# Performance work log

Hardware: AMD Instinct MI355X
Metric: run time of the kernel (lower is better)

The kernel has to match this reference:

```python
import jax, jax.numpy as jnp
import numpy as np

EPS = 1e-6
SIGMA = 1.0       # get_matrix default sigma
INIT_SIGMA = 1.0  # args.init_sigma


def setup_inputs() -> dict:
    key = jax.random.key(0)
    ks = jax.random.split(key, 12)
    B, T, LD, NB = 16, 2048, 256, 32
    s = 1.0 / np.sqrt(LD)
    E_raw = jax.random.normal(ks[5], (LD, LD), jnp.float32)
    E_w, _ = jnp.linalg.qr(E_raw)  # orthogonal like geotorch.orthogonal
    return {
        "Z": jax.random.normal(ks[0], (B, T, LD), jnp.float32),
        "obs_times": jax.random.uniform(ks[1], (B, T, 1), jnp.float32),
        "D": jax.random.normal(ks[2], (NB, LD), jnp.float32),
        "coeff_W": jax.random.normal(ks[3], (NB, LD), jnp.float32) * s,
        "coeff_b": jnp.zeros((NB,), jnp.float32),
        "E_w": E_w.astype(jnp.float32),
        "B_w": jax.random.normal(ks[6], (LD, LD), jnp.float32) * s,
        "C_w": jax.random.normal(ks[7], (LD, LD), jnp.float32) * s,
        "M_w": jax.random.normal(ks[8], (LD, LD), jnp.float32) * s,
        "init_mean_p": jax.random.normal(ks[9], (LD,), jnp.float32),
        "init_log_var": jax.random.normal(ks[10], (LD,), jnp.float32),
        "y_log_var": jax.random.normal(ks[11], (LD,), jnp.float32),
    }


def _binop(qi, qj):
    # (A_j*A_i, Bu_j + A_j*Bu_i): combine earlier element qi with later qj
    A_i, Bu_i = qi
    A_j, Bu_j = qj
    return (A_j * A_i, Bu_j + A_j * Bu_i)


def reference(Z, obs_times, D, coeff_W, coeff_b, E_w, B_w, C_w, M_w,
              init_mean_p, init_log_var, y_log_var):
    LD = Z.shape[-1]
    # alphas = B(Z)
    alphas = jnp.einsum('btd,ed->bte', Z, B_w)                      # (B,T,LD)
    # get_matrix (vectorized over batch and time)
    A_basis = -(jnp.exp(D) + EPS)                                   # (NB,LD), negative
    A_coeff = jax.nn.softmax(jnp.einsum('btd,nd->btn', alphas, coeff_W) + coeff_b, axis=-1)
    A_mat = jnp.einsum('btn,nd->btd', A_coeff, A_basis)             # (B,T,LD)
    exp_A_m = jnp.exp(A_mat * obs_times)                            # mean transition
    exp_B_m = (exp_A_m - 1.0) / A_mat * alphas
    exp_A_v = jnp.exp(2.0 * A_mat * obs_times)                      # var transition
    exp_B_v = 0.5 * SIGMA ** 2 * (exp_A_v - 1.0) / A_mat + EPS
    mats_A = jnp.concatenate([exp_A_m, exp_A_v], axis=-1)           # (B,T,2LD)
    mats_B = jnp.concatenate([exp_B_m, exp_B_v], axis=-1)           # (B,T,2LD)
    # parallel linear-recurrence scan over time
    cum_A, cum_B = jax.lax.associative_scan(_binop, (mats_A, mats_B), axis=1)
    # initial condition in rotated coordinates
    init_mean0 = E_w.T @ init_mean_p                                # (LD,)
    diag_v = INIT_SIGMA * (jnp.exp(init_log_var) + EPS)
    init_var0 = jnp.einsum('ki,k->i', E_w ** 2, diag_v)             # diag(E^T diag(v) E)
    init_mv = jnp.concatenate([init_mean0, init_var0], axis=0)      # (2LD,)
    imv = cum_A * init_mv                                           # (B,T,2LD)
    init_mean, init_var = imv[..., :LD], imv[..., LD:]
    xs_mean, xs_var = cum_B[..., :LD], cum_B[..., LD:]
    y_var = jnp.exp(y_log_var) + EPS
    # output projections: M(E(.)) and history C(E(Z))
    history = jnp.einsum('btd,ed,fe->btf', Z, E_w, C_w)
    means = jnp.einsum('btd,ed,fe->btf', xs_mean + init_mean, E_w, M_w) + history
    stds = jnp.einsum('btd,ed,fe->btf', jnp.sqrt(xs_var + init_var + y_var), E_w, M_w)
    return means, stds, alphas
```

## Files before the change

### kernel.cpp

```cpp
#include <hip/hip_runtime.h>
#include <math.h>

#define EPS 1e-6f

#define B_   16
#define T_   2048
#define LD   256
#define NB   32
#define BT   (B_ * T_)
#define NCH  32
#define CHUNK (T_ / NCH)

typedef short bf16x8 __attribute__((ext_vector_type(8)));
typedef float f32x4  __attribute__((ext_vector_type(4)));

__device__ __forceinline__ unsigned short f2b(float f) {
    unsigned int u = __float_as_uint(f);
    unsigned int r = (u + 0x7fffu + ((u >> 16) & 1u)) >> 16;
    return (unsigned short)r;
}

__device__ __forceinline__ void gl_lds16(const void* g, void* l) {
    __builtin_amdgcn_global_load_lds(
        (const __attribute__((address_space(1))) unsigned int*)g,
        (__attribute__((address_space(3))) unsigned int*)l, 16, 0, 0);
}

__device__ __forceinline__ void stage_tile(const unsigned short* __restrict__ src,
                                           int row0, int stride, int kb,
                                           unsigned short* lds, int wv, int lane) {
#pragma unroll
    for (int cc = 0; cc < 2; ++cc) {
        int c = wv * 2 + cc;
        int r = c * 16 + (lane >> 2);
        int qd = (lane & 3) ^ ((r >> 1) & 3);
        const unsigned short* g = src + (size_t)(row0 + r) * stride + kb + qd * 8;
        gl_lds16(g, lds + c * 512);
    }
}

__device__ __forceinline__ bf16x8 frag_ld(const unsigned short* lds, int row, int qd) {
    int pq = qd ^ ((row >> 1) & 3);
    return *(const bf16x8*)(lds + row * 32 + pq * 8);
}

template<int KLEN, int HALVES, int DUAL>
__global__ __launch_bounds__(256) void k_gemm128(const unsigned short* __restrict__ A0,
                                                 const unsigned short* __restrict__ A1,
                                                 const unsigned short* __restrict__ B0,
                                                 const unsigned short* __restrict__ B1,
                                                 float* __restrict__ C,
                                                 unsigned short* __restrict__ C2,
                                                 int nout) {
    __shared__ unsigned short As[128 * 32];
    __shared__ unsigned short Bs[128 * 32];
    int tid = threadIdx.x, lane = tid & 63, wv = tid >> 6;
    int m0 = blockIdx.x * 128, n0 = blockIdx.y * 128;
    int wm = (wv & 1) * 64, wn = (wv >> 1) * 64;
    f32x4 acc[4][4];
#pragma unroll
    for (int i = 0; i < 4; ++i)
#pragma unroll
        for (int j = 0; j < 4; ++j) acc[i][j] = (f32x4){0.f, 0.f, 0.f, 0.f};

    for (int h = 0; h < HALVES; ++h) {
        const unsigned short* A = h ? A1 : A0;
        const unsigned short* B = h ? B1 : B0;
        for (int kb = 0; kb < KLEN; kb += 32) {
            stage_tile(A, m0, KLEN, kb, As, wv, lane);
            stage_tile(B, n0, KLEN, kb, Bs, wv, lane);
            __syncthreads();
            int qd = lane >> 4;
            bf16x8 af[4], bf[4];
#pragma unroll
            for (int i = 0; i < 4; ++i) af[i] = frag_ld(As, wm + i * 16 + (lane & 15), qd);
#pragma unroll
            for (int j = 0; j < 4; ++j) bf[j] = frag_ld(Bs, wn + j * 16 + (lane & 15), qd);
#pragma unroll
            for (int i = 0; i < 4; ++i)
#pragma unroll
                for (int j = 0; j < 4; ++j)
                    acc[i][j] = __builtin_amdgcn_mfma_f32_16x16x32_bf16(af[i], bf[j], acc[i][j], 0, 0, 0);
            __syncthreads();
        }
    }
    int col = wn + (lane & 15);
    int rb  = wm + ((lane >> 4) << 2);
#pragma unroll
    for (int i = 0; i < 4; ++i)
#pragma unroll
        for (int j = 0; j < 4; ++j)
#pragma unroll
            for (int r = 0; r < 4; ++r) {
                int row = m0 + rb + i * 16 + r;
                int cc  = n0 + col + j * 16;
                float v = acc[i][j][r];
                C[(size_t)row * nout + cc] = v;
                if (DUAL) C2[(size_t)row * nout + cc] = f2b(v);
            }
}

__global__ __launch_bounds__(256) void k_gemm_logits(const unsigned short* __restrict__ A,
                                                     const unsigned short* __restrict__ B,
                                                     const float* __restrict__ bias,
                                                     float* __restrict__ C) {
    __shared__ unsigned short As[128 * 32];
    __shared__ unsigned short Bs2[32 * 32];
    int tid = threadIdx.x, lane = tid & 63, wv = tid >> 6;
    int m0 = blockIdx.x * 128;
    f32x4 acc[2][2];
#pragma unroll
    for (int i = 0; i < 2; ++i)
#pragma unroll
        for (int j = 0; j < 2; ++j) acc[i][j] = (f32x4){0.f, 0.f, 0.f, 0.f};

    for (int kb = 0; kb < 256; kb += 32) {
        stage_tile(A, m0, 256, kb, As, wv, lane);
        if (wv < 2) {
            int r = wv * 16 + (lane >> 2);
            int qd = (lane & 3) ^ ((r >> 1) & 3);
            gl_lds16(B + (size_t)r * 256 + kb + qd * 8, Bs2 + wv * 512);
        }
        __syncthreads();
        int qd = lane >> 4;
        bf16x8 af[2], bff[2];
#pragma unroll
        for (int i = 0; i < 2; ++i) af[i] = frag_ld(As, wv * 32 + i * 16 + (lane & 15), qd);
#pragma unroll
        for (int j = 0; j < 2; ++j) bff[j] = frag_ld(Bs2, j * 16 + (lane & 15), qd);
#pragma unroll
        for (int i = 0; i < 2; ++i)
#pragma unroll
            for (int j = 0; j < 2; ++j)
                acc[i][j] = __builtin_amdgcn_mfma_f32_16x16x32_bf16(af[i], bff[j], acc[i][j], 0, 0, 0);
        __syncthreads();
    }
    int col = lane & 15;
    int rb  = (lane >> 4) << 2;
#pragma unroll
    for (int i = 0; i < 2; ++i)
#pragma unroll
        for (int j = 0; j < 2; ++j)
#pragma unroll
            for (int r = 0; r < 4; ++r) {
                int row = m0 + wv * 32 + i * 16 + rb + r;
                int cc  = j * 16 + col;
                C[(size_t)row * NB + cc] = acc[i][j][r] + bias[cc];
            }
}

__global__ void k_cast(const float* __restrict__ src, unsigned short* __restrict__ dst, int n4) {
    int i = blockIdx.x * blockDim.x + threadIdx.x;
    if (i < n4) {
        float4 v = ((const float4*)src)[i];
        ushort4 o = make_ushort4(f2b(v.x), f2b(v.y), f2b(v.z), f2b(v.w));
        ((ushort4*)dst)[i] = o;
    }
}

__global__ void k_small_gemm(const float* __restrict__ E, const float* __restrict__ W,
                             unsigned short* __restrict__ out) {
    __shared__ float Ws[16][17];
    __shared__ float Es[16][17];
    int tx = threadIdx.x, ty = threadIdx.y;
    int d0 = blockIdx.x * 16, f0 = blockIdx.y * 16;
    float acc = 0.f;
    for (int eb = 0; eb < LD; eb += 16) {
        Ws[ty][tx] = W[(f0 + ty) * LD + eb + tx];
        Es[ty][tx] = E[(eb + ty) * LD + d0 + tx];
        __syncthreads();
#pragma unroll
        for (int k = 0; k < 16; ++k) acc = fmaf(Ws[ty][k], Es[k][tx], acc);
        __syncthreads();
    }
    out[(f0 + ty) * LD + d0 + tx] = f2b(acc);
}

__global__ void k_vec_pre(const float* __restrict__ E, const float* __restrict__ imp,
                          const float* __restrict__ ilv, const float* __restrict__ ylv,
                          const float* __restrict__ Dm,
                          float* __restrict__ im0, float* __restrict__ iv0,
                          float* __restrict__ yv, unsigned short* __restrict__ AbT) {
    int t = threadIdx.x;
    if (blockIdx.x == 0) {
        float sm = 0.f, sv = 0.f;
        for (int k = 0; k < LD; ++k) {
            float e = E[k * LD + t];
            sm = fmaf(e, imp[k], sm);
            sv = fmaf(e * e, expf(ilv[k]) + EPS, sv);
        }
        im0[t] = sm;
        iv0[t] = sv;
        yv[t]  = expf(ylv[t]) + EPS;
    } else {
        int n = blockIdx.x - 1;
        AbT[t * NB + n] = f2b(-(expf(Dm[n * LD + t]) + EPS));
    }
}

__global__ __launch_bounds__(256) void k_soft(const float* __restrict__ logits,
                                              unsigned short* __restrict__ ach) {
    int tid = threadIdx.x;
    int row = blockIdx.x * 8 + (tid >> 5);
    int l = tid & 31;
    float v = logits[(size_t)row * NB + l];
    float mx = v;
#pragma unroll
    for (int off = 16; off >= 1; off >>= 1) mx = fmaxf(mx, __shfl_xor(mx, off, 32));
    float e = expf(v - mx);
    float s = e;
#pragma unroll
    for (int off = 16; off >= 1; off >>= 1) s += __shfl_xor(s, off, 32);
    ach[(size_t)row * NB + l] = f2b(e / s);
}

__global__ __launch_bounds__(256) void k_tot(const float* __restrict__ Amat,
                                             const float* __restrict__ alphas,
                                             const float* __restrict__ obs,
                                             float* __restrict__ totA,
                                             float* __restrict__ totBm,
                                             float* __restrict__ totBv) {
    int d = threadIdx.x;
    int b = blockIdx.x >> 5, ch = blockIdx.x & 31;
    int bt0 = b * T_ + ch * CHUNK;
    float ra = 1.f, rm = 0.f, rv = 0.f;
    for (int i = 0; i < CHUNK; ++i) {
        size_t idx = (size_t)(bt0 + i) * LD + d;
        float Am = Amat[idx];
        float av = alphas[idx];
        float tt = obs[bt0 + i];
        float eAm = expf(Am * tt);
        float ieA = 1.f / Am;
        float eBm = (eAm - 1.f) * ieA * av;
        float eBv = 0.5f * (eAm * eAm - 1.f) * ieA + EPS;
        rm = fmaf(eAm, rm, eBm);
        rv = fmaf(eAm * eAm, rv, eBv);
        ra *= eAm;
    }
    int pidx = blockIdx.x * LD + d;
    totA[pidx] = ra; totBm[pidx] = rm; totBv[pidx] = rv;
}

__global__ void k_chunkpfx(const float* __restrict__ totA, const float* __restrict__ totBm,
                           const float* __restrict__ totBv,
                           float* __restrict__ preA, float* __restrict__ preBm,
                           float* __restrict__ preBv) {
    int d = threadIdx.x;
    int b = blockIdx.x;
    float Pa = 1.f, Pm = 0.f, Pv = 0.f;
    for (int ch = 0; ch < NCH; ++ch) {
        int pidx = (b * NCH + ch) * LD + d;
        preA[pidx] = Pa; preBm[pidx] = Pm; preBv[pidx] = Pv;
        float a = totA[pidx], tm_ = totBm[pidx], tv = totBv[pidx];
        Pm = fmaf(a, Pm, tm_);
        Pv = fmaf(a * a, Pv, tv);
        Pa = a * Pa;
    }
}

__global__ __launch_bounds__(256) void k_scan_apply(const float* __restrict__ Amat,
                                                    const float* __restrict__ alphas,
                                                    const float* __restrict__ obs,
                                                    const float* __restrict__ preA,
                                                    const float* __restrict__ preBm,
                                                    const float* __restrict__ preBv,
                                                    const float* __restrict__ im0,
                                                    const float* __restrict__ iv0,
                                                    const float* __restrict__ yv,
                                                    unsigned short* __restrict__ Mh,
                                                    unsigned short* __restrict__ Sh) {
    int d = threadIdx.x;
    int b = blockIdx.x >> 5, ch = blockIdx.x & 31;
    int bt0 = b * T_ + ch * CHUNK;
    int pidx = blockIdx.x * LD + d;
    float ga = preA[pidx], gm = preBm[pidx], gv = preBv[pidx];
    float i0 = im0[d], v0 = iv0[d], yvd = yv[d];
    for (int i = 0; i < CHUNK; ++i) {
        size_t idx = (size_t)(bt0 + i) * LD + d;
        float Am = Amat[idx];
        float av = alphas[idx];
        float tt = obs[bt0 + i];
        float eAm = expf(Am * tt);
        float ieA = 1.f / Am;
        float eBm = (eAm - 1.f) * ieA * av;
        float eBv = 0.5f * (eAm * eAm - 1.f) * ieA + EPS;
        gm = fmaf(eAm, gm, eBm);
        gv = fmaf(eAm * eAm, gv, eBv);
        ga *= eAm;
        float mm = fmaf(ga, i0, gm);
        float vv = fmaf(ga * ga, v0, gv) + yvd;
        Mh[idx] = f2b(mm);
        Sh[idx] = f2b(sqrtf(vv));
    }
}

extern "C" void kernel_launch(void* const* d_in, const int* in_sizes, int n_in,
                              void* d_out, int out_size, void* d_ws, size_t ws_size,
                              hipStream_t stream) {
    const float* Z   = (const float*)d_in[0];
    const float* obs = (const float*)d_in[1];
    const float* Dm  = (const float*)d_in[2];
    const float* cw  = (const float*)d_in[3];
    const float* cb  = (const float*)d_in[4];
    const float* Ew  = (const float*)d_in[5];
    const float* Bw  = (const float*)d_in[6];
    const float* Cw  = (const float*)d_in[7];
    const float* Mw  = (const float*)d_in[8];
    const float* imp = (const float*)d_in[9];
    const float* ilv = (const float*)d_in[10];
    const float* ylv = (const float*)d_in[11];

    float* out    = (float*)d_out;
    float* means  = out;
    float* stds   = out + (size_t)BT * LD;
    float* alphas = out + (size_t)2 * BT * LD;

    unsigned short* Zh = (unsigned short*)stds;

    char* ws = (char*)d_ws;
    size_t o = 0;
    float*          Amat = (float*)(ws + o);          o += (size_t)BT * LD * 4;
    unsigned short* Mh   = (unsigned short*)(ws + o); o += (size_t)BT * LD * 2;
    unsigned short* Sh   = (unsigned short*)(ws + o); o += (size_t)BT * LD * 2;
    unsigned short* ach  = (unsigned short*)(ws + o); o += (size_t)BT * NB * 2;
    unsigned short* GMh  = (unsigned short*)(ws + o); o += (size_t)LD * LD * 2;
    unsigned short* GCh  = (unsigned short*)(ws + o); o += (size_t)LD * LD * 2;
    unsigned short* Bwh  = (unsigned short*)(ws + o); o += (size_t)LD * LD * 2;
    unsigned short* cwh  = (unsigned short*)(ws + o); o += (size_t)NB * LD * 2;
    unsigned short* AbT  = (unsigned short*)(ws + o); o += (size_t)LD * NB * 2;
    float* totA  = (float*)(ws + o); o += (size_t)B_ * NCH * LD * 4;
    float* totBm = (float*)(ws + o); o += (size_t)B_ * NCH * LD * 4;
    float* totBv = (float*)(ws + o); o += (size_t)B_ * NCH * LD * 4;
    float* preA  = (float*)(ws + o); o += (size_t)B_ * NCH * LD * 4;
    float* preBm = (float*)(ws + o); o += (size_t)B_ * NCH * LD * 4;
    float* preBv = (float*)(ws + o); o += (size_t)B_ * NCH * LD * 4;
    float* im0   = (float*)(ws + o); o += LD * 4;
    float* iv0   = (float*)(ws + o); o += LD * 4;
    float* yv    = (float*)(ws + o); o += LD * 4;

    unsigned short* alphash = Mh;
    float*          logits  = (float*)Sh;

    k_cast<<<dim3((BT * LD / 4 + 255) / 256), dim3(256), 0, stream>>>(Z, Zh, BT * LD / 4);
    k_cast<<<dim3((LD * LD / 4 + 255) / 256), dim3(256), 0, stream>>>(Bw, Bwh, LD * LD / 4);
    k_cast<<<dim3((NB * LD / 4 + 255) / 256), dim3(256), 0, stream>>>(cw, cwh, NB * LD / 4);
    k_small_gemm<<<dim3(16, 16), dim3(16, 16), 0, stream>>>(Ew, Mw, GMh);
    k_small_gemm<<<dim3(16, 16), dim3(16, 16), 0, stream>>>(Ew, Cw, GCh);
    k_vec_pre<<<dim3(33), dim3(LD), 0, stream>>>(Ew, imp, ilv, ylv, Dm, im0, iv0, yv, AbT);

    k_gemm128<256, 1, 1><<<dim3(BT / 128, 2), dim3(256), 0, stream>>>(
        Zh, nullptr, Bwh, nullptr, alphas, alphash, LD);

    k_gemm_logits<<<dim3(BT / 128), dim3(256), 0, stream>>>(alphash, cwh, cb, logits);
    k_soft<<<dim3(BT / 8), dim3(256), 0, stream>>>(logits, ach);
    k_gemm128<32, 1, 0><<<dim3(BT / 128, 2), dim3(256), 0, stream>>>(
        ach, nullptr, AbT, nullptr, Amat, nullptr, LD);

    k_tot<<<dim3(B_ * NCH), dim3(LD), 0, stream>>>(Amat, alphas, obs, totA, totBm, totBv);
    k_chunkpfx<<<dim3(B_), dim3(LD), 0, stream>>>(totA, totBm, totBv, preA, preBm, preBv);
    k_scan_apply<<<dim3(B_ * NCH), dim3(LD), 0, stream>>>(Amat, alphas, obs,
                                                          preA, preBm, preBv,
                                                          im0, iv0, yv, Mh, Sh);

    k_gemm128<256, 2, 0><<<dim3(BT / 128, 2), dim3(256), 0, stream>>>(
        Mh, Zh, GMh, GCh, means, nullptr, LD);
    k_gemm128<256, 1, 0><<<dim3(BT / 128, 2), dim3(256), 0, stream>>>(
        Sh, nullptr, GMh, nullptr, stds, nullptr, LD);
}
```

Baseline: 288.9 us.

## Fold B_w into coeff_W, fuse prep kernels, recompute A_mat inside scan

Collapses the setup casts, small GEMMs and vector prep into one multi-role launch, and precomputes coeff_W·B_w so the logits come straight from Z. The logits GEMM then runs in the same launch as the alphas GEMM. Softmax and the A_mat contraction are recomputed in the two scan kernels from logits held in LDS, so the fp32 A_mat tensor is never written to or read from global memory. The means and stds GEMMs are merged into a single launch. This cuts launches and large intermediate traffic, at the cost of redundant softmax and 32-term dot products in each scan pass and a changed rounding path for the logits.

```diff
diff --git a/kernel.cpp b/kernel.cpp
--- a/kernel.cpp
+++ b/kernel.cpp
@@ -44,31 +44,95 @@
     return *(const bf16x8*)(lds + row * 32 + pq * 8);
 }
 
-template<int KLEN, int HALVES, int DUAL>
-__global__ __launch_bounds__(256) void k_gemm128(const unsigned short* __restrict__ A0,
-                                                 const unsigned short* __restrict__ A1,
-                                                 const unsigned short* __restrict__ B0,
-                                                 const unsigned short* __restrict__ B1,
-                                                 float* __restrict__ C,
-                                                 unsigned short* __restrict__ C2,
-                                                 int nout) {
+__global__ __launch_bounds__(256) void k_pre(const float* __restrict__ Z,
+                                             const float* __restrict__ Dm,
+                                             const float* __restrict__ cw,
+                                             const float* __restrict__ Ew,
+                                             const float* __restrict__ Bw,
+                                             const float* __restrict__ Cw,
+                                             const float* __restrict__ Mw,
+                                             const float* __restrict__ imp,
+                                             const float* __restrict__ ilv,
+                                             const float* __restrict__ ylv,
+                                             unsigned short* __restrict__ GMh,
+                                             unsigned short* __restrict__ GCh,
+                                             unsigned short* __restrict__ cwbh,
+                                             float* __restrict__ im0,
+                                             float* __restrict__ iv0,
+                                             float* __restrict__ yv,
+                                             float* __restrict__ Ab,
+                                             unsigned short* __restrict__ Bwh,
+                                             unsigned short* __restrict__ Zh) {
+    int bid = blockIdx.x;
+    int tid = threadIdx.x;
+    if (bid < 544) {
+        const float* W; const float* E; unsigned short* out; int d0, f0;
+        if (bid < 256)      { W = Mw; E = Ew; out = GMh;  d0 = (bid & 15) * 16; f0 = (bid >> 4) * 16; }
+        else if (bid < 512) { W = Cw; E = Ew; out = GCh;  d0 = (bid & 15) * 16; f0 = ((bid - 256) >> 4) * 16; }
+        else                { W = cw; E = Bw; out = cwbh; d0 = (bid & 15) * 16; f0 = ((bid - 512) >> 4) * 16; }
+        __shared__ float Ws[16][17];
+        __shared__ float Es[16][17];
+        int tx = tid & 15, ty = tid >> 4;
+        float acc = 0.f;
+        for (int eb = 0; eb < LD; eb += 16) {
+            Ws[ty][tx] = W[(f0 + ty) * LD + eb + tx];
+            Es[ty][tx] = E[(eb + ty) * LD + d0 + tx];
+            __syncthreads();
+#pragma unroll
+            for (int k = 0; k < 16; ++k) acc = fmaf(Ws[ty][k], Es[k][tx], acc);
+            __syncthreads();
+        }
+        out[(f0 + ty) * LD + d0 + tx] = f2b(acc);
+    } else if (bid < 577) {
+        int sub = bid - 544;
+        int t = tid;
+        if (sub == 0) {
+            float sm = 0.f, sv = 0.f;
+            for (int k = 0; k < LD; ++k) {
+                float e = Ew[k * LD + t];
+                sm = fmaf(e, imp[k], sm);
+                sv = fmaf(e * e, expf(ilv[k]) + EPS, sv);
+            }
+            im0[t] = sm;
+            iv0[t] = sv;
+            yv[t]  = expf(ylv[t]) + EPS;
+        } else {
+            int n = sub - 1;
+            Ab[n * LD + t] = -(expf(Dm[n * LD + t]) + EPS);
+        }
+    } else if (bid < 641) {
+        int i = (bid - 577) * 256 + tid;
+        float4 v = ((const float4*)Bw)[i];
+        ((ushort4*)Bwh)[i] = make_ushort4(f2b(v.x), f2b(v.y), f2b(v.z), f2b(v.w));
+    } else {
+        int i = (bid - 641) * 256 + tid;
+        float4 v = ((const float4*)Z)[i];
+        ((ushort4*)Zh)[i] = make_ushort4(f2b(v.x), f2b(v.y), f2b(v.z), f2b(v.w));
+    }
+}
+
+__global__ __launch_bounds__(256) void k_zb(const unsigned short* __restrict__ Zh,
+                                            const unsigned short* __restrict__ Bwh,
+                                            const unsigned short* __restrict__ cwbh,
+                                            const float* __restrict__ cb,
+                                            float* __restrict__ alphas,
+                                            float* __restrict__ logits) {
     __shared__ unsigned short As[128 * 32];
     __shared__ unsigned short Bs[128 * 32];
     int tid = threadIdx.x, lane = tid & 63, wv = tid >> 6;
-    int m0 = blockIdx.x * 128, n0 = blockIdx.y * 128;
-    int wm = (wv & 1) * 64, wn = (wv >> 1) * 64;
-    f32x4 acc[4][4];
-#pragma unroll
-    for (int i = 0; i < 4; ++i)
-#pragma unroll
-        for (int j = 0; j < 4; ++j) acc[i][j] = (f32x4){0.f, 0.f, 0.f, 0.f};
-
-    for (int h = 0; h < HALVES; ++h) {
-        const unsigned short* A = h ? A1 : A0;
-        const unsigned short* B = h ? B1 : B0;
-        for (int kb = 0; kb < KLEN; kb += 32) {
-            stage_tile(A, m0, KLEN, kb, As, wv, lane);
-            stage_tile(B, n0, KLEN, kb, Bs, wv, lane);
+    int m0 = blockIdx.x * 128;
+    int y  = blockIdx.y;
+    if (y < 2) {
+        int n0 = y * 128;
+        int wm = (wv & 1) * 64, wn = (wv >> 1) * 64;
+        f32x4 acc[4][4];
+#pragma unroll
+        for (int i = 0; i < 4; ++i)
+#pragma unroll
+            for (int j = 0; j < 4; ++j) acc[i][j] = (f32x4){0.f, 0.f, 0.f, 0.f};
+        for (int kb = 0; kb < LD; kb += 32) {
+            stage_tile(Zh, m0, LD, kb, As, wv, lane);
+            stage_tile(Bwh, n0, LD, kb, Bs, wv, lane);
             __syncthreads();
             int qd = lane >> 4;
             bf16x8 af[4], bf[4];
@@ -83,152 +147,109 @@
                     acc[i][j] = __builtin_amdgcn_mfma_f32_16x16x32_bf16(af[i], bf[j], acc[i][j], 0, 0, 0);
             __syncthreads();
         }
-    }
-    int col = wn + (lane & 15);
-    int rb  = wm + ((lane >> 4) << 2);
-#pragma unroll
-    for (int i = 0; i < 4; ++i)
-#pragma unroll
-        for (int j = 0; j < 4; ++j)
-#pragma unroll
-            for (int r = 0; r < 4; ++r) {
-                int row = m0 + rb + i * 16 + r;
-                int cc  = n0 + col + j * 16;
-                float v = acc[i][j][r];
-                C[(size_t)row * nout + cc] = v;
-                if (DUAL) C2[(size_t)row * nout + cc] = f2b(v);
+        int col = wn + (lane & 15);
+        int rb  = wm + ((lane >> 4) << 2);
+#pragma unroll
+        for (int i = 0; i < 4; ++i)
+#pragma unroll
+            for (int j = 0; j < 4; ++j)
+#pragma unroll
+                for (int r = 0; r < 4; ++r)
+                    alphas[(size_t)(m0 + rb + i * 16 + r) * LD + n0 + col + j * 16] = acc[i][j][r];
+    } else {
+        f32x4 acc[2][2];
+#pragma unroll
+        for (int i = 0; i < 2; ++i)
+#pragma unroll
+            for (int j = 0; j < 2; ++j) acc[i][j] = (f32x4){0.f, 0.f, 0.f, 0.f};
+        for (int kb = 0; kb < LD; kb += 32) {
+            stage_tile(Zh, m0, LD, kb, As, wv, lane);
+            if (wv < 2) {
+                int r = wv * 16 + (lane >> 2);
+                int qd = (lane & 3) ^ ((r >> 1) & 3);
+                gl_lds16(cwbh + (size_t)r * LD + kb + qd * 8, Bs + wv * 512);
             }
-}
-
-__global__ __launch_bounds__(256) void k_gemm_logits(const unsigned short* __restrict__ A,
-                                                     const unsigned short* __restrict__ B,
-                                                     const float* __restrict__ bias,
-                                                     float* __restrict__ C) {
-    __shared__ unsigned short As[128 * 32];
-    __shared__ unsigned short Bs2[32 * 32];
-    int tid = threadIdx.x, lane = tid & 63, wv = tid >> 6;
-    int m0 = blockIdx.x * 128;
-    f32x4 acc[2][2];
-#pragma unroll
-    for (int i = 0; i < 2; ++i)
-#pragma unroll
-        for (int j = 0; j < 2; ++j) acc[i][j] = (f32x4){0.f, 0.f, 0.f, 0.f};
-
-    for (int kb = 0; kb < 256; kb += 32) {
-        stage_tile(A, m0, 256, kb, As, wv, lane);
-        if (wv < 2) {
-            int r = wv * 16 + (lane >> 2);
-            int qd = (lane & 3) ^ ((r >> 1) & 3);
-            gl_lds16(B + (size_t)r * 256 + kb + qd * 8, Bs2 + wv * 512);
+            __syncthreads();
+            int qd = lane >> 4;
+            bf16x8 af[2], bff[2];
+#pragma unroll
+            for (int i = 0; i < 2; ++i) af[i] = frag_ld(As, wv * 32 + i * 16 + (lane & 15), qd);
+#pragma unroll
+            for (int j = 0; j < 2; ++j) bff[j] = frag_ld(Bs, j * 16 + (lane & 15), qd);
+#pragma unroll
+            for (int i = 0; i < 2; ++i)
+#pragma unroll
+                for (int j = 0; j < 2; ++j)
+                    acc[i][j] = __builtin_amdgcn_mfma_f32_16x16x32_bf16(af[i], bff[j], acc[i][j], 0, 0, 0);
+            __syncthreads();
         }
-        __syncthreads();
-        int qd = lane >> 4;
-        bf16x8 af[2], bff[2];
-#pragma unroll
-        for (int i = 0; i < 2; ++i) af[i] = frag_ld(As, wv * 32 + i * 16 + (lane & 15), qd);
-#pragma unroll
-        for (int j = 0; j < 2; ++j) bff[j] = frag_ld(Bs2, j * 16 + (lane & 15), qd);
+        int col = lane & 15;
+        int rb  = (lane >> 4) << 2;
 #pragma unroll
         for (int i = 0; i < 2; ++i)
 #pragma unroll
             for (int j = 0; j < 2; ++j)
-                acc[i][j] = __builtin_amdgcn_mfma_f32_16x16x32_bf16(af[i], bff[j], acc[i][j], 0, 0, 0);
-        __syncthreads();
-    }
-    int col = lane & 15;
-    int rb  = (lane >> 4) << 2;
-#pragma unroll
-    for (int i = 0; i < 2; ++i)
-#pragma unroll
-        for (int j = 0; j < 2; ++j)
-#pragma unroll
-            for (int r = 0; r < 4; ++r) {
-                int row = m0 + wv * 32 + i * 16 + rb + r;
-                int cc  = j * 16 + col;
-                C[(size_t)row * NB + cc] = acc[i][j][r] + bias[cc];
-            }
-}
-
-__global__ void k_cast(const float* __restrict__ src, unsigned short* __restrict__ dst, int n4) {
-    int i = blockIdx.x * blockDim.x + threadIdx.x;
-    if (i < n4) {
-        float4 v = ((const float4*)src)[i];
-        ushort4 o = make_ushort4(f2b(v.x), f2b(v.y), f2b(v.z), f2b(v.w));
-        ((ushort4*)dst)[i] = o;
-    }
-}
-
-__global__ void k_small_gemm(const float* __restrict__ E, const float* __restrict__ W,
-                             unsigned short* __restrict__ out) {
-    __shared__ float Ws[16][17];
-    __shared__ float Es[16][17];
-    int tx = threadIdx.x, ty = threadIdx.y;
-    int d0 = blockIdx.x * 16, f0 = blockIdx.y * 16;
-    float acc = 0.f;
-    for (int eb = 0; eb < LD; eb += 16) {
-        Ws[ty][tx] = W[(f0 + ty) * LD + eb + tx];
-        Es[ty][tx] = E[(eb + ty) * LD + d0 + tx];
-        __syncthreads();
-#pragma unroll
-        for (int k = 0; k < 16; ++k) acc = fmaf(Ws[ty][k], Es[k][tx], acc);
-        __syncthreads();
-    }
-    out[(f0 + ty) * LD + d0 + tx] = f2b(acc);
-}
-
-__global__ void k_vec_pre(const float* __restrict__ E, const float* __restrict__ imp,
-                          const float* __restrict__ ilv, const float* __restrict__ ylv,
-                          const float* __restrict__ Dm,
-                          float* __restrict__ im0, float* __restrict__ iv0,
-                          float* __restrict__ yv, unsigned short* __restrict__ AbT) {
-    int t = threadIdx.x;
-    if (blockIdx.x == 0) {
-        float sm = 0.f, sv = 0.f;
-        for (int k = 0; k < LD; ++k) {
-            float e = E[k * LD + t];
-            sm = fmaf(e, imp[k], sm);
-            sv = fmaf(e * e, expf(ilv[k]) + EPS, sv);
-        }
-        im0[t] = sm;
-        iv0[t] = sv;
-        yv[t]  = expf(ylv[t]) + EPS;
-    } else {
-        int n = blockIdx.x - 1;
-        AbT[t * NB + n] = f2b(-(expf(Dm[n * LD + t]) + EPS));
-    }
-}
-
-__global__ __launch_bounds__(256) void k_soft(const float* __restrict__ logits,
-                                              unsigned short* __restrict__ ach) {
+#pragma unroll
+                for (int r = 0; r < 4; ++r) {
+                    int row = m0 + wv * 32 + i * 16 + rb + r;
+                    int cc  = j * 16 + col;
+                    logits[(size_t)row * NB + cc] = acc[i][j][r] + cb[cc];
+                }
+    }
+}
+
+__device__ __forceinline__ void scan_prolog(const float* __restrict__ logits,
+                                            const float* __restrict__ obs,
+                                            const float* __restrict__ Ab,
+                                            int bt0, int d,
+                                            float (*lg)[NB], float* obs_s, float* abc) {
     int tid = threadIdx.x;
-    int row = blockIdx.x * 8 + (tid >> 5);
-    int l = tid & 31;
-    float v = logits[(size_t)row * NB + l];
-    float mx = v;
-#pragma unroll
-    for (int off = 16; off >= 1; off >>= 1) mx = fmaxf(mx, __shfl_xor(mx, off, 32));
-    float e = expf(v - mx);
-    float s = e;
-#pragma unroll
-    for (int off = 16; off >= 1; off >>= 1) s += __shfl_xor(s, off, 32);
-    ach[(size_t)row * NB + l] = f2b(e / s);
-}
-
-__global__ __launch_bounds__(256) void k_tot(const float* __restrict__ Amat,
+    float4* lg4 = (float4*)lg;
+    const float4* g4 = (const float4*)(logits + (size_t)bt0 * NB);
+    lg4[tid]       = g4[tid];
+    lg4[tid + 256] = g4[tid + 256];
+    if (tid < CHUNK) obs_s[tid] = obs[bt0 + tid];
+    __syncthreads();
+    int l = tid & 31, rg = tid >> 5;
+#pragma unroll
+    for (int j = 0; j < 8; ++j) {
+        int row = rg * 8 + j;
+        float v = lg[row][l];
+        float mx = v;
+#pragma unroll
+        for (int off = 16; off >= 1; off >>= 1) mx = fmaxf(mx, __shfl_xor(mx, off, 32));
+        float e = expf(v - mx);
+        float s = e;
+#pragma unroll
+        for (int off = 16; off >= 1; off >>= 1) s += __shfl_xor(s, off, 32);
+        lg[row][l] = e / s;
+    }
+    __syncthreads();
+#pragma unroll
+    for (int n = 0; n < NB; ++n) abc[n] = Ab[n * LD + d];
+}
+
+__global__ __launch_bounds__(256) void k_tot(const float* __restrict__ logits,
                                              const float* __restrict__ alphas,
                                              const float* __restrict__ obs,
+                                             const float* __restrict__ Ab,
                                              float* __restrict__ totA,
                                              float* __restrict__ totBm,
                                              float* __restrict__ totBv) {
+    __shared__ float lg[CHUNK][NB];
+    __shared__ float obs_s[CHUNK];
     int d = threadIdx.x;
     int b = blockIdx.x >> 5, ch = blockIdx.x & 31;
     int bt0 = b * T_ + ch * CHUNK;
+    float abc[NB];
+    scan_prolog(logits, obs, Ab, bt0, d, lg, obs_s, abc);
     float ra = 1.f, rm = 0.f, rv = 0.f;
     for (int i = 0; i < CHUNK; ++i) {
-        size_t idx = (size_t)(bt0 + i) * LD + d;
-        float Am = Amat[idx];
-        float av = alphas[idx];
-        float tt = obs[bt0 + i];
+        float av = alphas[(size_t)(bt0 + i) * LD + d];
+        float Am = 0.f;
+#pragma unroll
+        for (int n = 0; n < NB; ++n) Am = fmaf(lg[i][n], abc[n], Am);
+        float tt  = obs_s[i];
         float eAm = expf(Am * tt);
         float ieA = 1.f / Am;
         float eBm = (eAm - 1.f) * ieA * av;
@@ -258,9 +279,10 @@
     }
 }
 
-__global__ __launch_bounds__(256) void k_scan_apply(const float* __restrict__ Amat,
+__global__ __launch_bounds__(256) void k_scan_apply(const float* __restrict__ logits,
                                                     const float* __restrict__ alphas,
                                                     const float* __restrict__ obs,
+                                                    const float* __restrict__ Ab,
                                                     const float* __restrict__ preA,
                                                     const float* __restrict__ preBm,
                                                     const float* __restrict__ preBv,
@@ -269,17 +291,23 @@
                                                     const float* __restrict__ yv,
                                                     unsigned short* __restrict__ Mh,
                                                     unsigned short* __restrict__ Sh) {
+    __shared__ float lg[CHUNK][NB];
+    __shared__ float obs_s[CHUNK];
     int d = threadIdx.x;
     int b = blockIdx.x >> 5, ch = blockIdx.x & 31;
     int bt0 = b * T_ + ch * CHUNK;
+    float abc[NB];
+    scan_prolog(logits, obs, Ab, bt0, d, lg, obs_s, abc);
     int pidx = blockIdx.x * LD + d;
     float ga = preA[pidx], gm = preBm[pidx], gv = preBv[pidx];
     float i0 = im0[d], v0 = iv0[d], yvd = yv[d];
     for (int i = 0; i < CHUNK; ++i) {
         size_t idx = (size_t)(bt0 + i) * LD + d;
-        float Am = Amat[idx];
         float av = alphas[idx];
-        float tt = obs[bt0 + i];
+        float Am = 0.f;
+#pragma unroll
+        for (int n = 0; n < NB; ++n) Am = fmaf(lg[i][n], abc[n], Am);
+        float tt  = obs_s[i];
         float eAm = expf(Am * tt);
         float ieA = 1.f / Am;
         float eBm = (eAm - 1.f) * ieA * av;
@@ -292,6 +320,63 @@
         Mh[idx] = f2b(mm);
         Sh[idx] = f2b(sqrtf(vv));
     }
+}
+
+__global__ __launch_bounds__(256) void k_ms(const unsigned short* __restrict__ Mh,
+                                            const unsigned short* __restrict__ Zh,
+                                            const unsigned short* __restrict__ Sh,
+                                            const unsigned short* __restrict__ GMh,
+                                            const unsigned short* __restrict__ GCh,
+                                            float* __restrict__ means,
+                                            float* __restrict__ stds) {
+    __shared__ unsigned short As[128 * 32];
+    __shared__ unsigned short Bs[128 * 32];
+    int tid = threadIdx.x, lane = tid & 63, wv = tid >> 6;
+    int m0 = blockIdx.x * 128;
+    int y  = blockIdx.y;
+    int halves = (y < 2) ? 2 : 1;
+    int n0 = (y < 2) ? y * 128 : (y - 2) * 128;
+    const unsigned short* A0 = (y < 2) ? Mh : Sh;
+    const unsigned short* A1 = Zh;
+    const unsigned short* B0 = GMh;
+    const unsigned short* B1 = GCh;
+    float* C = (y < 2) ? means : stds;
+    int wm = (wv & 1) * 64, wn = (wv >> 1) * 64;
+    f32x4 acc[4][4];
+#pragma unroll
+    for (int i = 0; i < 4; ++i)
+#pragma unroll
+        for (int j = 0; j < 4; ++j) acc[i][j] = (f32x4){0.f, 0.f, 0.f, 0.f};
+    for (int h = 0; h < halves; ++h) {
+        const unsigned short* A = h ? A1 : A0;
+        const unsigned short* B = h ? B1 : B0;
+        for (int kb = 0; kb < LD; kb += 32) {
+            stage_tile(A, m0, LD, kb, As, wv, lane);
+            stage_tile(B, n0, LD, kb, Bs, wv, lane);
+            __syncthreads();
+            int qd = lane >> 4;
+            bf16x8 af[4], bf[4];
+#pragma unroll
+            for (int i = 0; i < 4; ++i) af[i] = frag_ld(As, wm + i * 16 + (lane & 15), qd);
+#pragma unroll
+            for (int j = 0; j < 4; ++j) bf[j] = frag_ld(Bs, wn + j * 16 + (lane & 15), qd);
+#pragma unroll
+            for (int i = 0; i < 4; ++i)
+#pragma unroll
+                for (int j = 0; j < 4; ++j)
+                    acc[i][j] = __builtin_amdgcn_mfma_f32_16x16x32_bf16(af[i], bf[j], acc[i][j], 0, 0, 0);
+            __syncthreads();
+        }
+    }
+    int col = wn + (lane & 15);
+    int rb  = wm + ((lane >> 4) << 2);
+#pragma unroll
+    for (int i = 0; i < 4; ++i)
+#pragma unroll
+        for (int j = 0; j < 4; ++j)
+#pragma unroll
+            for (int r = 0; r < 4; ++r)
+                C[(size_t)(m0 + rb + i * 16 + r) * LD + n0 + col + j * 16] = acc[i][j][r];
 }
 
 extern "C" void kernel_launch(void* const* d_in, const int* in_sizes, int n_in,
@@ -315,19 +400,17 @@
     float* stds   = out + (size_t)BT * LD;
     float* alphas = out + (size_t)2 * BT * LD;
 
-    unsigned short* Zh = (unsigned short*)stds;
-
     char* ws = (char*)d_ws;
     size_t o = 0;
-    float*          Amat = (float*)(ws + o);          o += (size_t)BT * LD * 4;
+    unsigned short* Zh   = (unsigned short*)(ws + o); o += (size_t)BT * LD * 2;
     unsigned short* Mh   = (unsigned short*)(ws + o); o += (size_t)BT * LD * 2;
     unsigned short* Sh   = (unsigned short*)(ws + o); o += (size_t)BT * LD * 2;
-    unsigned short* ach  = (unsigned short*)(ws + o); o += (size_t)BT * NB * 2;
+    float*          logits=(float*)(ws + o);          o += (size_t)BT * NB * 4;
     unsigned short* GMh  = (unsigned short*)(ws + o); o += (size_t)LD * LD * 2;
     unsigned short* GCh  = (unsigned short*)(ws + o); o += (size_t)LD * LD * 2;
     unsigned short* Bwh  = (unsigned short*)(ws + o); o += (size_t)LD * LD * 2;
-    unsigned short* cwh  = (unsigned short*)(ws + o); o += (size_t)NB * LD * 2;
-    unsigned short* AbT  = (unsigned short*)(ws + o); o += (size_t)LD * NB * 2;
+    unsigned short* cwbh = (unsigned short*)(ws + o); o += (size_t)NB * LD * 2;
+    float* Ab    = (float*)(ws + o); o += (size_t)NB * LD * 4;
     float* totA  = (float*)(ws + o); o += (size_t)B_ * NCH * LD * 4;
     float* totBm = (float*)(ws + o); o += (size_t)B_ * NCH * LD * 4;
     float* totBv = (float*)(ws + o); o += (size_t)B_ * NCH * LD * 4;
@@ -338,32 +421,17 @@
     float* iv0   = (float*)(ws + o); o += LD * 4;
     float* yv    = (float*)(ws + o); o += LD * 4;
 
-    unsigned short* alphash = Mh;
-    float*          logits  = (float*)Sh;
-
-    k_cast<<<dim3((BT * LD / 4 + 255) / 256), dim3(256), 0, stream>>>(Z, Zh, BT * LD / 4);
-    k_cast<<<dim3((LD * LD / 4 + 255) / 256), dim3(256), 0, stream>>>(Bw, Bwh, LD * LD / 4);
-    k_cast<<<dim3((NB * LD / 4 + 255) / 256), dim3(256), 0, stream>>>(cw, cwh, NB * LD / 4);
-    k_small_gemm<<<dim3(16, 16), dim3(16, 16), 0, stream>>>(Ew, Mw, GMh);
-    k_small_gemm<<<dim3(16, 16), dim3(16, 16), 0, stream>>>(Ew, Cw, GCh);
-    k_vec_pre<<<dim3(33), dim3(LD), 0, stream>>>(Ew, imp, ilv, ylv, Dm, im0, iv0, yv, AbT);
-
-    k_gemm128<256, 1, 1><<<dim3(BT / 128, 2), dim3(256), 0, stream>>>(
-        Zh, nullptr, Bwh, nullptr, alphas, alphash, LD);
-
-    k_gemm_logits<<<dim3(BT / 128), dim3(256), 0, stream>>>(alphash, cwh, cb, logits);
-    k_soft<<<dim3(BT / 8), dim3(256), 0, stream>>>(logits, ach);
-    k_gemm128<32, 1, 0><<<dim3(BT / 128, 2), dim3(256), 0, stream>>>(
-        ach, nullptr, AbT, nullptr, Amat, nullptr, LD);
-
-    k_tot<<<dim3(B_ * NCH), dim3(LD), 0, stream>>>(Amat, alphas, obs, totA, totBm, totBv);
+    k_pre<<<dim3(641 + BT * LD / 1024), dim3(256), 0, stream>>>(
+        Z, Dm, cw, Ew, Bw, Cw, Mw, imp, ilv, ylv,
+        GMh, GCh, cwbh, im0, iv0, yv, Ab, Bwh, Zh);
+
+    k_zb<<<dim3(BT / 128, 3), dim3(256), 0, stream>>>(Zh, Bwh, cwbh, cb, alphas, logits);
+
+    k_tot<<<dim3(B_ * NCH), dim3(LD), 0, stream>>>(logits, alphas, obs, Ab, totA, totBm, totBv);
     k_chunkpfx<<<dim3(B_), dim3(LD), 0, stream>>>(totA, totBm, totBv, preA, preBm, preBv);
-    k_scan_apply<<<dim3(B_ * NCH), dim3(LD), 0, stream>>>(Amat, alphas, obs,
+    k_scan_apply<<<dim3(B_ * NCH), dim3(LD), 0, stream>>>(logits, alphas, obs, Ab,
                                                           preA, preBm, preBv,
                                                           im0, iv0, yv, Mh, Sh);
 
-    k_gemm128<256, 2, 0><<<dim3(BT / 128, 2), dim3(256), 0, stream>>>(
-        Mh, Zh, GMh, GCh, means, nullptr, LD);
-    k_gemm128<256, 1, 0><<<dim3(BT / 128, 2), dim3(256), 0, stream>>>(
-        Sh, nullptr, GMh, nullptr, stds, nullptr, LD);
-}
+    k_ms<<<dim3(BT / 128, 4), dim3(256), 0, stream>>>(Mh, Zh, Sh, GMh, GCh, means, stds);
+}
```

Measured after the change: 249.3 us. -13.7%, faster.
